# Kernel optimization log

Hardware: AMD Instinct MI355X
Metric: run time of the kernel (lower is better)

The kernel has to match this reference:

```python
import jax, jax.numpy as jnp
import numpy as np

NEG_INF = -1.0e9  # matches torch masked_fill value (unused: no mask)

def setup_inputs() -> dict:
    key = jax.random.key(0)
    kq, kk, kv = jax.random.split(key, 3)
    B, Sq, Sk, D = 8, 2048, 2048, 512
    return {
        "query": jax.random.normal(kq, (B, Sq, D), dtype=jnp.float32),
        "key": jax.random.normal(kk, (B, Sk, D), dtype=jnp.float32),
        "value": jax.random.normal(kv, (B, Sk, D), dtype=jnp.float32),
        "temperature": jnp.ones((), dtype=jnp.float32),
    }

def reference(query, key, value, temperature):
    # Squared Euclidean distance via GEMM identity: ||q||^2 + ||k||^2 - 2 q.k
    # (same math as the broadcast sum((q-k)^2, -1), but without [B,Sq,Sk,D] tensor)
    q_sq = jnp.sum(query * query, axis=-1, keepdims=True)          # [B,Sq,1]
    k_sq = jnp.sum(key * key, axis=-1)[:, None, :]                 # [B,1,Sk]
    qk = jnp.einsum("bqd,bkd->bqk", query, key)                    # [B,Sq,Sk]
    distance_squared = q_sq + k_sq - 2.0 * qk
    similarity = -distance_squared / temperature
    attention_weights = jax.nn.softmax(similarity, axis=-1)        # [B,Sq,Sk]
    attended_values = jnp.einsum("bqk,bkd->bqd", attention_weights, value)
    return attended_values, attention_weights
```

## Files before the change

kernel.cpp:

```cpp
#include <hip/hip_runtime.h>

typedef __bf16 bf16_t;
typedef __bf16 bf16x8 __attribute__((ext_vector_type(8)));
typedef __bf16 bf16x4 __attribute__((ext_vector_type(4)));
typedef __bf16 bf16x2 __attribute__((ext_vector_type(2)));
typedef float f32x4 __attribute__((ext_vector_type(4)));

#define NB 8
#define SQ 2048
#define SK 2048
#define DD 512

#define BM 128
#define BN 128
#define BK 32
#define LDK 40
#define NBLK (SK / BN)

__global__ __launch_bounds__(256, 2) void logits_kernel(
    const float* __restrict__ Q, const float* __restrict__ K,
    const float* __restrict__ tempP, float* __restrict__ logits,
    float* __restrict__ Mpart, float* __restrict__ Spart) {
  __shared__ bf16_t qh[BM][LDK], ql[BM][LDK], kh[BN][LDK], kl[BN][LDK];
  __shared__ float ksred[BN][8];
  __shared__ float mred[BM][2], sred[BM][2];
  const int b = blockIdx.z;
  const int m0 = blockIdx.y * BM;
  const int n0 = blockIdx.x * BN;
  const int tid = threadIdx.x;
  const int lane = tid & 63;
  const int wave = tid >> 6;
  const int wm = (wave >> 1) * 64;
  const int wn = (wave & 1) * 64;
  const int lrow = lane & 15;
  const int quad = lane >> 4;

  const float* Qb = Q + (size_t)b * SQ * DD;
  const float* Kb = K + (size_t)b * SK * DD;

  const int srow = tid >> 3;
  const int scol = (tid & 7) * 4;

  const float* qbase = Qb + (size_t)(m0 + srow) * DD + scol;
  const float* kbase = Kb + (size_t)(n0 + srow) * DD + scol;

  f32x4 acc[4][4];
#pragma unroll
  for (int i = 0; i < 4; i++)
#pragma unroll
    for (int j = 0; j < 4; j++) acc[i][j] = (f32x4){0.f, 0.f, 0.f, 0.f};

  float kss[4] = {0.f, 0.f, 0.f, 0.f};

  float4 pq[4], pk[4];
#pragma unroll
  for (int i = 0; i < 4; i++) {
    pq[i] = *(const float4*)(qbase + (size_t)i * 32 * DD);
    pk[i] = *(const float4*)(kbase + (size_t)i * 32 * DD);
  }

  for (int k0 = 0; k0 < DD; k0 += BK) {
    __syncthreads();
#pragma unroll
    for (int i = 0; i < 4; i++) {
      const int r = srow + i * 32;
      float4 qv = pq[i], kv = pk[i];
      bf16_t q0 = (bf16_t)qv.x, q1 = (bf16_t)qv.y, q2 = (bf16_t)qv.z, q3 = (bf16_t)qv.w;
      bf16x4 qhv = {q0, q1, q2, q3};
      bf16x4 qlv = {(bf16_t)(qv.x - (float)q0), (bf16_t)(qv.y - (float)q1),
                    (bf16_t)(qv.z - (float)q2), (bf16_t)(qv.w - (float)q3)};
      bf16_t c0 = (bf16_t)kv.x, c1 = (bf16_t)kv.y, c2 = (bf16_t)kv.z, c3 = (bf16_t)kv.w;
      bf16x4 khv = {c0, c1, c2, c3};
      bf16x4 klv = {(bf16_t)(kv.x - (float)c0), (bf16_t)(kv.y - (float)c1),
                    (bf16_t)(kv.z - (float)c2), (bf16_t)(kv.w - (float)c3)};
      *(bf16x4*)&qh[r][scol] = qhv;
      *(bf16x4*)&ql[r][scol] = qlv;
      *(bf16x4*)&kh[r][scol] = khv;
      *(bf16x4*)&kl[r][scol] = klv;
      kss[i] = fmaf(kv.x, kv.x, kss[i]);
      kss[i] = fmaf(kv.y, kv.y, kss[i]);
      kss[i] = fmaf(kv.z, kv.z, kss[i]);
      kss[i] = fmaf(kv.w, kv.w, kss[i]);
    }
    __syncthreads();

    if (k0 + BK < DD) {
#pragma unroll
      for (int i = 0; i < 4; i++) {
        pq[i] = *(const float4*)(qbase + (size_t)i * 32 * DD + (k0 + BK));
        pk[i] = *(const float4*)(kbase + (size_t)i * 32 * DD + (k0 + BK));
      }
    }

    bf16x8 bh[4], bl[4];
#pragma unroll
    for (int ni = 0; ni < 4; ni++) {
      bh[ni] = *(const bf16x8*)&kh[wn + ni * 16 + lrow][quad * 8];
      bl[ni] = *(const bf16x8*)&kl[wn + ni * 16 + lrow][quad * 8];
    }
#pragma unroll
    for (int mi = 0; mi < 4; mi++) {
      bf16x8 ah = *(const bf16x8*)&qh[wm + mi * 16 + lrow][quad * 8];
      bf16x8 al = *(const bf16x8*)&ql[wm + mi * 16 + lrow][quad * 8];
#pragma unroll
      for (int ni = 0; ni < 4; ni++) {
        acc[mi][ni] = __builtin_amdgcn_mfma_f32_16x16x32_bf16(ah, bh[ni], acc[mi][ni], 0, 0, 0);
        acc[mi][ni] = __builtin_amdgcn_mfma_f32_16x16x32_bf16(ah, bl[ni], acc[mi][ni], 0, 0, 0);
        acc[mi][ni] = __builtin_amdgcn_mfma_f32_16x16x32_bf16(al, bh[ni], acc[mi][ni], 0, 0, 0);
      }
    }
  }

#pragma unroll
  for (int i = 0; i < 4; i++) ksred[srow + i * 32][tid & 7] = kss[i];
  __syncthreads();

  const float invT = 1.4426950408889634f / tempP[0];
  float* Lb = logits + (size_t)b * SQ * SK;
  float ks4[4];
#pragma unroll
  for (int ni = 0; ni < 4; ni++) {
    const float* kr = ksred[wn + ni * 16 + lrow];
    ks4[ni] = ((kr[0] + kr[1]) + (kr[2] + kr[3])) +
              ((kr[4] + kr[5]) + (kr[6] + kr[7]));
  }

#pragma unroll
  for (int mi = 0; mi < 4; mi++) {
#pragma unroll
    for (int r = 0; r < 4; r++) {
      const int row = wm + mi * 16 + quad * 4 + r;
      float sv[4];
#pragma unroll
      for (int ni = 0; ni < 4; ni++) {
        sv[ni] = (2.0f * acc[mi][ni][r] - ks4[ni]) * invT;
        Lb[(size_t)(m0 + row) * SK + (n0 + wn + ni * 16 + lrow)] = sv[ni];
      }
      float rm = fmaxf(fmaxf(sv[0], sv[1]), fmaxf(sv[2], sv[3]));
      rm = fmaxf(rm, __shfl_xor(rm, 1));
      rm = fmaxf(rm, __shfl_xor(rm, 2));
      rm = fmaxf(rm, __shfl_xor(rm, 4));
      rm = fmaxf(rm, __shfl_xor(rm, 8));
      float rs = exp2f(sv[0] - rm) + exp2f(sv[1] - rm) +
                 exp2f(sv[2] - rm) + exp2f(sv[3] - rm);
      rs += __shfl_xor(rs, 1);
      rs += __shfl_xor(rs, 2);
      rs += __shfl_xor(rs, 4);
      rs += __shfl_xor(rs, 8);
      if (lrow == 0) {
        mred[row][wave & 1] = rm;
        sred[row][wave & 1] = rs;
      }
    }
  }
  __syncthreads();
  if (tid < BM) {
    const float ma = mred[tid][0], mb = mred[tid][1];
    const float M = fmaxf(ma, mb);
    const float S = sred[tid][0] * exp2f(ma - M) + sred[tid][1] * exp2f(mb - M);
    const size_t o = ((size_t)b * NBLK + blockIdx.x) * SQ + (m0 + tid);
    Mpart[o] = M;
    Spart[o] = S;
  }
}

__global__ __launch_bounds__(256) void vt_kernel(const float* __restrict__ V,
                                                 bf16_t* __restrict__ Vt) {
  const int b = blockIdx.y;
  const int k0 = blockIdx.x * 32;
  const int tid = threadIdx.x;
  const int p = tid & 15;
  const int c = tid >> 4;
  const float* Vb = V + (size_t)b * SK * DD;
  bf16_t* Vtb = Vt + (size_t)b * DD * SK;
  const int k = k0 + 2 * p;
#pragma unroll
  for (int j = 0; j < 8; j++) {
    const int d0 = 4 * c + 64 * j;
    float4 v0 = *(const float4*)(Vb + (size_t)k * DD + d0);
    float4 v1 = *(const float4*)(Vb + (size_t)(k + 1) * DD + d0);
    bf16x2 t0 = {(bf16_t)v0.x, (bf16_t)v1.x};
    bf16x2 t1 = {(bf16_t)v0.y, (bf16_t)v1.y};
    bf16x2 t2 = {(bf16_t)v0.z, (bf16_t)v1.z};
    bf16x2 t3 = {(bf16_t)v0.w, (bf16_t)v1.w};
    *(bf16x2*)(Vtb + (size_t)(d0 + 0) * SK + k) = t0;
    *(bf16x2*)(Vtb + (size_t)(d0 + 1) * SK + k) = t1;
    *(bf16x2*)(Vtb + (size_t)(d0 + 2) * SK + k) = t2;
    *(bf16x2*)(Vtb + (size_t)(d0 + 3) * SK + k) = t3;
  }
}

#define PM 32
#define CK 256
#define CKB 512
#define NCH (SK / CK)
#define NWIN (SK / BK)

__device__ __forceinline__ unsigned pv_lds(int row, unsigned kb) {
  return (unsigned)row * CKB + (kb ^ (unsigned)((row & 7) << 4));
}

__global__ __launch_bounds__(512, 4) void pv_kernel(
    float* __restrict__ L,
    const bf16_t* __restrict__ Vt,
    const float* __restrict__ Mpart, const float* __restrict__ Spart,
    float* __restrict__ O) {
  __shared__ __align__(16) unsigned char wlds[2][PM * CKB];
  __shared__ float Msh[PM], Ssh[PM];
  const int bid = blockIdx.x;
  const int b = bid & 7;
  const int m0 = (bid >> 3) * PM;
  const int tid = threadIdx.x;

  float* Lb = L + (size_t)b * SQ * SK;
  const bf16_t* Vtb = Vt + (size_t)b * DD * SK;

  {
    const int row = tid >> 4;
    const int j = tid & 15;
    const size_t o = ((size_t)b * NBLK + j) * SQ + (m0 + row);
    const float pm = Mpart[o];
    const float ps = Spart[o];
    float m = pm;
    m = fmaxf(m, __shfl_xor(m, 1));
    m = fmaxf(m, __shfl_xor(m, 2));
    m = fmaxf(m, __shfl_xor(m, 4));
    m = fmaxf(m, __shfl_xor(m, 8));
    float s = ps * exp2f(pm - m);
    s += __shfl_xor(s, 1);
    s += __shfl_xor(s, 2);
    s += __shfl_xor(s, 4);
    s += __shfl_xor(s, 8);
    if (j == 0) {
      Msh[row] = m;
      Ssh[row] = 1.0f / s;
    }
  }
  __syncthreads();

  const int prow = tid >> 4;
  const int g = tid & 15;
  float* lp = Lb + (size_t)(m0 + prow) * SK;
  const float Mrow = Msh[prow];
  const float invS = Ssh[prow];

  auto stage = [&](const float4 (&pv4)[4], int c1) {
    unsigned char* buf = wlds[c1 & 1];
    const int kbase = c1 * CK;
#pragma unroll
    for (int j = 0; j < 4; j++) {
      const int k = g * 4 + j * 64;
      float4 v = pv4[j];
      const float w0 = exp2f(v.x - Mrow) * invS;
      const float w1 = exp2f(v.y - Mrow) * invS;
      const float w2 = exp2f(v.z - Mrow) * invS;
      const float w3 = exp2f(v.w - Mrow) * invS;
      *(float4*)(lp + kbase + k) = make_float4(w0, w1, w2, w3);
      bf16x4 w4 = {(bf16_t)w0, (bf16_t)w1, (bf16_t)w2, (bf16_t)w3};
      *(bf16x4*)(buf + pv_lds(prow, (unsigned)(k * 2))) = w4;
    }
  };

  const int lane = tid & 63;
  const int wave = tid >> 6;
  const int wn = wave * 64;
  const int lrow = lane & 15;
  const int quad = lane >> 4;

  const bf16_t* Brow[4];
#pragma unroll
  for (int ni = 0; ni < 4; ni++)
    Brow[ni] = Vtb + (size_t)(wn + ni * 16 + lrow) * SK + quad * 8;

  f32x4 acc[2][4];
#pragma unroll
  for (int i = 0; i < 2; i++)
#pragma unroll
    for (int j = 0; j < 4; j++) acc[i][j] = (f32x4){0.f, 0.f, 0.f, 0.f};

  {
    float4 p0[4];
#pragma unroll
    for (int j = 0; j < 4; j++) p0[j] = *(const float4*)(lp + g * 4 + j * 64);
    stage(p0, 0);
  }
  bf16x8 bw[2][4];
#pragma unroll
  for (int ni = 0; ni < 4; ni++) bw[0][ni] = *(const bf16x8*)(Brow[ni]);
#pragma unroll
  for (int ni = 0; ni < 4; ni++) bw[1][ni] = *(const bf16x8*)(Brow[ni] + BK);
  __syncthreads();

  for (int c = 0; c < NCH; c++) {
    float4 pn[4];
    if (c + 1 < NCH) {
      const int kbase = (c + 1) * CK;
#pragma unroll
      for (int j = 0; j < 4; j++)
        pn[j] = *(const float4*)(lp + kbase + g * 4 + j * 64);
    }

    const unsigned char* buf = wlds[c & 1];
#pragma unroll
    for (int w = 0; w < CK / BK; w++) {
      const int gw = c * (CK / BK) + w;
      bf16x8 a0 = *(const bf16x8*)(buf + pv_lds(lrow, (unsigned)(w * 64 + quad * 16)));
      bf16x8 a1 = *(const bf16x8*)(buf + pv_lds(16 + lrow, (unsigned)(w * 64 + quad * 16)));
#pragma unroll
      for (int ni = 0; ni < 4; ni++)
        acc[0][ni] = __builtin_amdgcn_mfma_f32_16x16x32_bf16(a0, bw[gw & 1][ni],
                                                             acc[0][ni], 0, 0, 0);
#pragma unroll
      for (int ni = 0; ni < 4; ni++)
        acc[1][ni] = __builtin_amdgcn_mfma_f32_16x16x32_bf16(a1, bw[gw & 1][ni],
                                                             acc[1][ni], 0, 0, 0);
      if (gw + 2 < NWIN) {
#pragma unroll
        for (int ni = 0; ni < 4; ni++)
          bw[gw & 1][ni] = *(const bf16x8*)(Brow[ni] + (gw + 2) * BK);
      }
    }

    if (c + 1 < NCH) {
      stage(pn, c + 1);
      asm volatile("s_waitcnt lgkmcnt(0)\n\ts_barrier" ::: "memory");
    }
  }

  float* Ob = O + (size_t)b * SQ * DD;
#pragma unroll
  for (int ni = 0; ni < 4; ni++) {
    const int d = wn + ni * 16 + lrow;
#pragma unroll
    for (int mi = 0; mi < 2; mi++) {
      const int mbase = m0 + mi * 16 + quad * 4;
#pragma unroll
      for (int r = 0; r < 4; r++) {
        Ob[(size_t)(mbase + r) * DD + d] = acc[mi][ni][r];
      }
    }
  }
}

extern "C" void kernel_launch(void* const* d_in, const int* in_sizes, int n_in,
                              void* d_out, int out_size, void* d_ws, size_t ws_size,
                              hipStream_t stream) {
  const float* Q = (const float*)d_in[0];
  const float* K = (const float*)d_in[1];
  const float* V = (const float*)d_in[2];
  const float* T = (const float*)d_in[3];

  float* outv = (float*)d_out;
  float* logits = outv + (size_t)NB * SQ * DD;

  float* Mpart = (float*)d_ws;
  float* Spart = Mpart + (size_t)NB * NBLK * SQ;
  bf16_t* Vt = (bf16_t*)(Spart + (size_t)NB * NBLK * SQ);

  vt_kernel<<<dim3(SK / 32, NB), 256, 0, stream>>>(V, Vt);
  logits_kernel<<<dim3(SK / BN, SQ / BM, NB), 256, 0, stream>>>(Q, K, T, logits,
                                                                Mpart, Spart);
  pv_kernel<<<dim3(NB * (SQ / PM)), 512, 0, stream>>>(logits, Vt, Mpart, Spart, outv);
}
```

Before: 460.0 us.

## Pre-pack Q/K into bf16 hi/lo rows and deepen P·V logits prefetch

Adds a pack kernel that splits Q and K once into bf16 hi/lo halves in a workspace and precomputes the K row norms. The logits GEMM then streams the packed bf16 data as a single K-extended dimension of 1536 (hi·hi, hi·lo, lo·hi), instead of reloading fp32 and re-splitting it in every tile. This removes the conversion work repeated across the 16 tile columns and halves the bytes loaded per element, at the cost of an extra kernel and workspace traffic. The P·V kernel now prefetches logits two chunks ahead and unrolls the V window double-buffer into explicit registers.

```diff
diff --git a/kernel.cpp b/kernel.cpp
--- a/kernel.cpp
+++ b/kernel.cpp
@@ -10,6 +10,8 @@
 #define SQ 2048
 #define SK 2048
 #define DD 512
+#define KP2 1024
+#define KV 1536
 
 #define BM 128
 #define BN 128
@@ -17,12 +19,48 @@
 #define LDK 40
 #define NBLK (SK / BN)
 
+__global__ __launch_bounds__(256) void pack_kernel(
+    const float* __restrict__ Q, const float* __restrict__ K,
+    bf16_t* __restrict__ QP, bf16_t* __restrict__ KP, float* __restrict__ Ksq) {
+  const int row = blockIdx.x * 4 + (threadIdx.x >> 6);
+  const int lane = threadIdx.x & 63;
+  const float* q = Q + (size_t)row * DD;
+  const float* k = K + (size_t)row * DD;
+  bf16_t* qp = QP + (size_t)row * KP2;
+  bf16_t* kp = KP + (size_t)row * KP2;
+  float ks = 0.f;
+#pragma unroll
+  for (int j = 0; j < 2; j++) {
+    const int c = lane * 4 + j * 256;
+    float4 qv = *(const float4*)(q + c);
+    float4 kv = *(const float4*)(k + c);
+    bf16_t q0 = (bf16_t)qv.x, q1 = (bf16_t)qv.y, q2 = (bf16_t)qv.z, q3 = (bf16_t)qv.w;
+    bf16x4 qh = {q0, q1, q2, q3};
+    bf16x4 ql = {(bf16_t)(qv.x - (float)q0), (bf16_t)(qv.y - (float)q1),
+                 (bf16_t)(qv.z - (float)q2), (bf16_t)(qv.w - (float)q3)};
+    bf16_t c0 = (bf16_t)kv.x, c1 = (bf16_t)kv.y, c2 = (bf16_t)kv.z, c3 = (bf16_t)kv.w;
+    bf16x4 kh = {c0, c1, c2, c3};
+    bf16x4 kl = {(bf16_t)(kv.x - (float)c0), (bf16_t)(kv.y - (float)c1),
+                 (bf16_t)(kv.z - (float)c2), (bf16_t)(kv.w - (float)c3)};
+    *(bf16x4*)(qp + c) = qh;
+    *(bf16x4*)(qp + 512 + c) = ql;
+    *(bf16x4*)(kp + c) = kh;
+    *(bf16x4*)(kp + 512 + c) = kl;
+    ks = fmaf(kv.x, kv.x, ks);
+    ks = fmaf(kv.y, kv.y, ks);
+    ks = fmaf(kv.z, kv.z, ks);
+    ks = fmaf(kv.w, kv.w, ks);
+  }
+#pragma unroll
+  for (int off = 32; off; off >>= 1) ks += __shfl_xor(ks, off);
+  if (lane == 0) Ksq[row] = ks;
+}
+
 __global__ __launch_bounds__(256, 2) void logits_kernel(
-    const float* __restrict__ Q, const float* __restrict__ K,
-    const float* __restrict__ tempP, float* __restrict__ logits,
-    float* __restrict__ Mpart, float* __restrict__ Spart) {
-  __shared__ bf16_t qh[BM][LDK], ql[BM][LDK], kh[BN][LDK], kl[BN][LDK];
-  __shared__ float ksred[BN][8];
+    const bf16_t* __restrict__ QP, const bf16_t* __restrict__ KPp,
+    const float* __restrict__ Ksq, const float* __restrict__ tempP,
+    float* __restrict__ logits, float* __restrict__ Mpart, float* __restrict__ Spart) {
+  __shared__ bf16_t at[BM][LDK], bt[BN][LDK];
   __shared__ float mred[BM][2], sred[BM][2];
   const int b = blockIdx.z;
   const int m0 = blockIdx.y * BM;
@@ -35,14 +73,11 @@
   const int lrow = lane & 15;
   const int quad = lane >> 4;
 
-  const float* Qb = Q + (size_t)b * SQ * DD;
-  const float* Kb = K + (size_t)b * SK * DD;
-
-  const int srow = tid >> 3;
-  const int scol = (tid & 7) * 4;
-
-  const float* qbase = Qb + (size_t)(m0 + srow) * DD + scol;
-  const float* kbase = Kb + (size_t)(n0 + srow) * DD + scol;
+  const int srow = tid >> 1;
+  const int k8 = (tid & 1) * 8;
+
+  const bf16_t* qbase = QP + ((size_t)b * SQ + m0 + srow) * KP2 + k8;
+  const bf16_t* kbase = KPp + ((size_t)b * SK + n0 + srow) * KP2 + k8;
 
   f32x4 acc[4][4];
 #pragma unroll
@@ -50,80 +85,48 @@
 #pragma unroll
     for (int j = 0; j < 4; j++) acc[i][j] = (f32x4){0.f, 0.f, 0.f, 0.f};
 
-  float kss[4] = {0.f, 0.f, 0.f, 0.f};
-
-  float4 pq[4], pk[4];
-#pragma unroll
-  for (int i = 0; i < 4; i++) {
-    pq[i] = *(const float4*)(qbase + (size_t)i * 32 * DD);
-    pk[i] = *(const float4*)(kbase + (size_t)i * 32 * DD);
-  }
-
-  for (int k0 = 0; k0 < DD; k0 += BK) {
+  bf16x8 pa0 = *(const bf16x8*)(qbase);
+  bf16x8 pa1 = *(const bf16x8*)(qbase + 16);
+  bf16x8 pb0 = *(const bf16x8*)(kbase);
+  bf16x8 pb1 = *(const bf16x8*)(kbase + 16);
+
+  for (int kv = 0; kv < KV; kv += BK) {
     __syncthreads();
-#pragma unroll
-    for (int i = 0; i < 4; i++) {
-      const int r = srow + i * 32;
-      float4 qv = pq[i], kv = pk[i];
-      bf16_t q0 = (bf16_t)qv.x, q1 = (bf16_t)qv.y, q2 = (bf16_t)qv.z, q3 = (bf16_t)qv.w;
-      bf16x4 qhv = {q0, q1, q2, q3};
-      bf16x4 qlv = {(bf16_t)(qv.x - (float)q0), (bf16_t)(qv.y - (float)q1),
-                    (bf16_t)(qv.z - (float)q2), (bf16_t)(qv.w - (float)q3)};
-      bf16_t c0 = (bf16_t)kv.x, c1 = (bf16_t)kv.y, c2 = (bf16_t)kv.z, c3 = (bf16_t)kv.w;
-      bf16x4 khv = {c0, c1, c2, c3};
-      bf16x4 klv = {(bf16_t)(kv.x - (float)c0), (bf16_t)(kv.y - (float)c1),
-                    (bf16_t)(kv.z - (float)c2), (bf16_t)(kv.w - (float)c3)};
-      *(bf16x4*)&qh[r][scol] = qhv;
-      *(bf16x4*)&ql[r][scol] = qlv;
-      *(bf16x4*)&kh[r][scol] = khv;
-      *(bf16x4*)&kl[r][scol] = klv;
-      kss[i] = fmaf(kv.x, kv.x, kss[i]);
-      kss[i] = fmaf(kv.y, kv.y, kss[i]);
-      kss[i] = fmaf(kv.z, kv.z, kss[i]);
-      kss[i] = fmaf(kv.w, kv.w, kss[i]);
-    }
+    *(bf16x8*)&at[srow][k8] = pa0;
+    *(bf16x8*)&at[srow][k8 + 16] = pa1;
+    *(bf16x8*)&bt[srow][k8] = pb0;
+    *(bf16x8*)&bt[srow][k8 + 16] = pb1;
     __syncthreads();
 
-    if (k0 + BK < DD) {
-#pragma unroll
-      for (int i = 0; i < 4; i++) {
-        pq[i] = *(const float4*)(qbase + (size_t)i * 32 * DD + (k0 + BK));
-        pk[i] = *(const float4*)(kbase + (size_t)i * 32 * DD + (k0 + BK));
-      }
-    }
-
-    bf16x8 bh[4], bl[4];
-#pragma unroll
-    for (int ni = 0; ni < 4; ni++) {
-      bh[ni] = *(const bf16x8*)&kh[wn + ni * 16 + lrow][quad * 8];
-      bl[ni] = *(const bf16x8*)&kl[wn + ni * 16 + lrow][quad * 8];
-    }
+    if (kv + BK < KV) {
+      const int kn = kv + BK;
+      const int ao = (kn < 512) ? kn : kn - 512;
+      const int bo = (kn < 1024) ? kn : kn - 1024;
+      pa0 = *(const bf16x8*)(qbase + ao);
+      pa1 = *(const bf16x8*)(qbase + ao + 16);
+      pb0 = *(const bf16x8*)(kbase + bo);
+      pb1 = *(const bf16x8*)(kbase + bo + 16);
+    }
+
+    bf16x8 bfr[4];
+#pragma unroll
+    for (int ni = 0; ni < 4; ni++)
+      bfr[ni] = *(const bf16x8*)&bt[wn + ni * 16 + lrow][quad * 8];
 #pragma unroll
     for (int mi = 0; mi < 4; mi++) {
-      bf16x8 ah = *(const bf16x8*)&qh[wm + mi * 16 + lrow][quad * 8];
-      bf16x8 al = *(const bf16x8*)&ql[wm + mi * 16 + lrow][quad * 8];
-#pragma unroll
-      for (int ni = 0; ni < 4; ni++) {
-        acc[mi][ni] = __builtin_amdgcn_mfma_f32_16x16x32_bf16(ah, bh[ni], acc[mi][ni], 0, 0, 0);
-        acc[mi][ni] = __builtin_amdgcn_mfma_f32_16x16x32_bf16(ah, bl[ni], acc[mi][ni], 0, 0, 0);
-        acc[mi][ni] = __builtin_amdgcn_mfma_f32_16x16x32_bf16(al, bh[ni], acc[mi][ni], 0, 0, 0);
-      }
-    }
-  }
-
-#pragma unroll
-  for (int i = 0; i < 4; i++) ksred[srow + i * 32][tid & 7] = kss[i];
-  __syncthreads();
+      bf16x8 a = *(const bf16x8*)&at[wm + mi * 16 + lrow][quad * 8];
+#pragma unroll
+      for (int ni = 0; ni < 4; ni++)
+        acc[mi][ni] = __builtin_amdgcn_mfma_f32_16x16x32_bf16(a, bfr[ni], acc[mi][ni], 0, 0, 0);
+    }
+  }
 
   const float invT = 1.4426950408889634f / tempP[0];
   float* Lb = logits + (size_t)b * SQ * SK;
+  const float* ksb = Ksq + (size_t)b * SK + n0;
   float ks4[4];
 #pragma unroll
-  for (int ni = 0; ni < 4; ni++) {
-    const float* kr = ksred[wn + ni * 16 + lrow];
-    ks4[ni] = ((kr[0] + kr[1]) + (kr[2] + kr[3])) +
-              ((kr[4] + kr[5]) + (kr[6] + kr[7]));
-  }
+  for (int ni = 0; ni < 4; ni++) ks4[ni] = ksb[wn + ni * 16 + lrow];
 
 #pragma unroll
   for (int mi = 0; mi < 4; mi++) {
@@ -284,47 +287,68 @@
     for (int j = 0; j < 4; j++) p0[j] = *(const float4*)(lp + g * 4 + j * 64);
     stage(p0, 0);
   }
-  bf16x8 bw[2][4];
-#pragma unroll
-  for (int ni = 0; ni < 4; ni++) bw[0][ni] = *(const bf16x8*)(Brow[ni]);
-#pragma unroll
-  for (int ni = 0; ni < 4; ni++) bw[1][ni] = *(const bf16x8*)(Brow[ni] + BK);
+  float4 pA[4];
+#pragma unroll
+  for (int j = 0; j < 4; j++) pA[j] = *(const float4*)(lp + CK + g * 4 + j * 64);
+
+  bf16x8 bw0[4], bw1[4];
+#pragma unroll
+  for (int ni = 0; ni < 4; ni++) bw0[ni] = *(const bf16x8*)(Brow[ni]);
+#pragma unroll
+  for (int ni = 0; ni < 4; ni++) bw1[ni] = *(const bf16x8*)(Brow[ni] + BK);
   __syncthreads();
 
   for (int c = 0; c < NCH; c++) {
-    float4 pn[4];
+    float4 pB_[4] = {};
+    if (c + 2 < NCH) {
+      const int kbase = (c + 2) * CK;
+#pragma unroll
+      for (int j = 0; j < 4; j++)
+        pB_[j] = *(const float4*)(lp + kbase + g * 4 + j * 64);
+    }
+
+    const unsigned char* buf = wlds[c & 1];
+#pragma unroll
+    for (int w = 0; w < CK / BK; w += 2) {
+      const int gw = c * (CK / BK) + w;
+      {
+        bf16x8 a0 = *(const bf16x8*)(buf + pv_lds(lrow, (unsigned)(w * 64 + quad * 16)));
+        bf16x8 a1 = *(const bf16x8*)(buf + pv_lds(16 + lrow, (unsigned)(w * 64 + quad * 16)));
+#pragma unroll
+        for (int ni = 0; ni < 4; ni++)
+          acc[0][ni] = __builtin_amdgcn_mfma_f32_16x16x32_bf16(a0, bw0[ni], acc[0][ni], 0, 0, 0);
+#pragma unroll
+        for (int ni = 0; ni < 4; ni++)
+          acc[1][ni] = __builtin_amdgcn_mfma_f32_16x16x32_bf16(a1, bw0[ni], acc[1][ni], 0, 0, 0);
+        if (gw + 2 < NWIN) {
+#pragma unroll
+          for (int ni = 0; ni < 4; ni++)
+            bw0[ni] = *(const bf16x8*)(Brow[ni] + (gw + 2) * BK);
+        }
+      }
+      {
+        bf16x8 a0 = *(const bf16x8*)(buf + pv_lds(lrow, (unsigned)((w + 1) * 64 + quad * 16)));
+        bf16x8 a1 = *(const bf16x8*)(buf + pv_lds(16 + lrow, (unsigned)((w + 1) * 64 + quad * 16)));
+#pragma unroll
+        for (int ni = 0; ni < 4; ni++)
+          acc[0][ni] = __builtin_amdgcn_mfma_f32_16x16x32_bf16(a0, bw1[ni], acc[0][ni], 0, 0, 0);
+#pragma unroll
+        for (int ni = 0; ni < 4; ni++)
+          acc[1][ni] = __builtin_amdgcn_mfma_f32_16x16x32_bf16(a1, bw1[ni], acc[1][ni], 0, 0, 0);
+        if (gw + 3 < NWIN) {
+#pragma unroll
+          for (int ni = 0; ni < 4; ni++)
+            bw1[ni] = *(const bf16x8*)(Brow[ni] + (gw + 3) * BK);
+        }
+      }
+    }
+
     if (c + 1 < NCH) {
-      const int kbase = (c + 1) * CK;
-#pragma unroll
-      for (int j = 0; j < 4; j++)
-        pn[j] = *(const float4*)(lp + kbase + g * 4 + j * 64);
-    }
-
-    const unsigned char* buf = wlds[c & 1];
-#pragma unroll
-    for (int w = 0; w < CK / BK; w++) {
-      const int gw = c * (CK / BK) + w;
-      bf16x8 a0 = *(const bf16x8*)(buf + pv_lds(lrow, (unsigned)(w * 64 + quad * 16)));
-      bf16x8 a1 = *(const bf16x8*)(buf + pv_lds(16 + lrow, (unsigned)(w * 64 + quad * 16)));
-#pragma unroll
-      for (int ni = 0; ni < 4; ni++)
-        acc[0][ni] = __builtin_amdgcn_mfma_f32_16x16x32_bf16(a0, bw[gw & 1][ni],
-                                                             acc[0][ni], 0, 0, 0);
-#pragma unroll
-      for (int ni = 0; ni < 4; ni++)
-        acc[1][ni] = __builtin_amdgcn_mfma_f32_16x16x32_bf16(a1, bw[gw & 1][ni],
-                                                             acc[1][ni], 0, 0, 0);
-      if (gw + 2 < NWIN) {
-#pragma unroll
-        for (int ni = 0; ni < 4; ni++)
-          bw[gw & 1][ni] = *(const bf16x8*)(Brow[ni] + (gw + 2) * BK);
-      }
-    }
-
-    if (c + 1 < NCH) {
-      stage(pn, c + 1);
+      stage(pA, c + 1);
       asm volatile("s_waitcnt lgkmcnt(0)\n\ts_barrier" ::: "memory");
     }
+#pragma unroll
+    for (int j = 0; j < 4; j++) pA[j] = pB_[j];
   }
 
   float* Ob = O + (size_t)b * SQ * DD;
@@ -356,9 +380,13 @@
   float* Mpart = (float*)d_ws;
   float* Spart = Mpart + (size_t)NB * NBLK * SQ;
   bf16_t* Vt = (bf16_t*)(Spart + (size_t)NB * NBLK * SQ);
-
+  bf16_t* QP = Vt + (size_t)NB * DD * SK;
+  bf16_t* KPp = QP + (size_t)NB * SQ * KP2;
+  float* Ksq = (float*)(KPp + (size_t)NB * SK * KP2);
+
+  pack_kernel<<<NB * SQ / 4, 256, 0, stream>>>(Q, K, QP, KPp, Ksq);
   vt_kernel<<<dim3(SK / 32, NB), 256, 0, stream>>>(V, Vt);
-  logits_kernel<<<dim3(SK / BN, SQ / BM, NB), 256, 0, stream>>>(Q, K, T, logits,
-                                                                Mpart, Spart);
+  logits_kernel<<<dim3(SK / BN, SQ / BM, NB), 256, 0, stream>>>(QP, KPp, Ksq, T,
+                                                                logits, Mpart, Spart);
   pv_kernel<<<dim3(NB * (SQ / PM)), 512, 0, stream>>>(logits, Vt, Mpart, Spart, outv);
 }
```

New measurement: 510.0 us. 10.9% more time.

## Drop V transpose kernel and partial softmax stats; convert V in-kernel and recompute stats

Applied to the files above, without the earlier changes.

Removes the separate V transpose/bf16 conversion kernel and the per-block max/sum partials from the logits kernel. The PV kernel now first re-reads each logits row to compute the online softmax max and sum itself. It then loads fp32 V tiles per 32-key window, converts and transposes them into a padded LDS buffer, and feeds them to MFMA. This saves a launch, the Vt workspace round trip and the epilogue reductions. In exchange it adds an extra full read of the logits, with each block re-reading and converting all of V. It also adds two barriers per 32-key window.

```diff
diff --git a/kernel.cpp b/kernel.cpp
--- a/kernel.cpp
+++ b/kernel.cpp
@@ -15,15 +15,12 @@
 #define BN 128
 #define BK 32
 #define LDK 40
-#define NBLK (SK / BN)
 
 __global__ __launch_bounds__(256, 2) void logits_kernel(
     const float* __restrict__ Q, const float* __restrict__ K,
-    const float* __restrict__ tempP, float* __restrict__ logits,
-    float* __restrict__ Mpart, float* __restrict__ Spart) {
+    const float* __restrict__ tempP, float* __restrict__ logits) {
   __shared__ bf16_t qh[BM][LDK], ql[BM][LDK], kh[BN][LDK], kl[BN][LDK];
   __shared__ float ksred[BN][8];
-  __shared__ float mred[BM][2], sred[BM][2];
   const int b = blockIdx.z;
   const int m0 = blockIdx.y * BM;
   const int n0 = blockIdx.x * BN;
@@ -130,63 +127,12 @@
 #pragma unroll
     for (int r = 0; r < 4; r++) {
       const int row = wm + mi * 16 + quad * 4 + r;
-      float sv[4];
 #pragma unroll
       for (int ni = 0; ni < 4; ni++) {
-        sv[ni] = (2.0f * acc[mi][ni][r] - ks4[ni]) * invT;
-        Lb[(size_t)(m0 + row) * SK + (n0 + wn + ni * 16 + lrow)] = sv[ni];
-      }
-      float rm = fmaxf(fmaxf(sv[0], sv[1]), fmaxf(sv[2], sv[3]));
-      rm = fmaxf(rm, __shfl_xor(rm, 1));
-      rm = fmaxf(rm, __shfl_xor(rm, 2));
-      rm = fmaxf(rm, __shfl_xor(rm, 4));
-      rm = fmaxf(rm, __shfl_xor(rm, 8));
-      float rs = exp2f(sv[0] - rm) + exp2f(sv[1] - rm) +
-                 exp2f(sv[2] - rm) + exp2f(sv[3] - rm);
-      rs += __shfl_xor(rs, 1);
-      rs += __shfl_xor(rs, 2);
-      rs += __shfl_xor(rs, 4);
-      rs += __shfl_xor(rs, 8);
-      if (lrow == 0) {
-        mred[row][wave & 1] = rm;
-        sred[row][wave & 1] = rs;
-      }
-    }
-  }
-  __syncthreads();
-  if (tid < BM) {
-    const float ma = mred[tid][0], mb = mred[tid][1];
-    const float M = fmaxf(ma, mb);
-    const float S = sred[tid][0] * exp2f(ma - M) + sred[tid][1] * exp2f(mb - M);
-    const size_t o = ((size_t)b * NBLK + blockIdx.x) * SQ + (m0 + tid);
-    Mpart[o] = M;
-    Spart[o] = S;
-  }
-}
-
-__global__ __launch_bounds__(256) void vt_kernel(const float* __restrict__ V,
-                                                 bf16_t* __restrict__ Vt) {
-  const int b = blockIdx.y;
-  const int k0 = blockIdx.x * 32;
-  const int tid = threadIdx.x;
-  const int p = tid & 15;
-  const int c = tid >> 4;
-  const float* Vb = V + (size_t)b * SK * DD;
-  bf16_t* Vtb = Vt + (size_t)b * DD * SK;
-  const int k = k0 + 2 * p;
-#pragma unroll
-  for (int j = 0; j < 8; j++) {
-    const int d0 = 4 * c + 64 * j;
-    float4 v0 = *(const float4*)(Vb + (size_t)k * DD + d0);
-    float4 v1 = *(const float4*)(Vb + (size_t)(k + 1) * DD + d0);
-    bf16x2 t0 = {(bf16_t)v0.x, (bf16_t)v1.x};
-    bf16x2 t1 = {(bf16_t)v0.y, (bf16_t)v1.y};
-    bf16x2 t2 = {(bf16_t)v0.z, (bf16_t)v1.z};
-    bf16x2 t3 = {(bf16_t)v0.w, (bf16_t)v1.w};
-    *(bf16x2*)(Vtb + (size_t)(d0 + 0) * SK + k) = t0;
-    *(bf16x2*)(Vtb + (size_t)(d0 + 1) * SK + k) = t1;
-    *(bf16x2*)(Vtb + (size_t)(d0 + 2) * SK + k) = t2;
-    *(bf16x2*)(Vtb + (size_t)(d0 + 3) * SK + k) = t3;
+        float sv = (2.0f * acc[mi][ni][r] - ks4[ni]) * invT;
+        Lb[(size_t)(m0 + row) * SK + (n0 + wn + ni * 16 + lrow)] = sv;
+      }
+    }
   }
 }
 
@@ -194,7 +140,7 @@
 #define CK 256
 #define CKB 512
 #define NCH (SK / CK)
-#define NWIN (SK / BK)
+#define LDV 40
 
 __device__ __forceinline__ unsigned pv_lds(int row, unsigned kb) {
   return (unsigned)row * CKB + (kb ^ (unsigned)((row & 7) << 4));
@@ -202,10 +148,10 @@
 
 __global__ __launch_bounds__(512, 4) void pv_kernel(
     float* __restrict__ L,
-    const bf16_t* __restrict__ Vt,
-    const float* __restrict__ Mpart, const float* __restrict__ Spart,
+    const float* __restrict__ V,
     float* __restrict__ O) {
   __shared__ __align__(16) unsigned char wlds[2][PM * CKB];
+  __shared__ __align__(16) bf16_t vwin[DD][LDV];
   __shared__ float Msh[PM], Ssh[PM];
   const int bid = blockIdx.x;
   const int b = bid & 7;
@@ -213,44 +159,55 @@
   const int tid = threadIdx.x;
 
   float* Lb = L + (size_t)b * SQ * SK;
-  const bf16_t* Vtb = Vt + (size_t)b * DD * SK;
-
-  {
-    const int row = tid >> 4;
-    const int j = tid & 15;
-    const size_t o = ((size_t)b * NBLK + j) * SQ + (m0 + row);
-    const float pm = Mpart[o];
-    const float ps = Spart[o];
-    float m = pm;
-    m = fmaxf(m, __shfl_xor(m, 1));
-    m = fmaxf(m, __shfl_xor(m, 2));
-    m = fmaxf(m, __shfl_xor(m, 4));
-    m = fmaxf(m, __shfl_xor(m, 8));
-    float s = ps * exp2f(pm - m);
-    s += __shfl_xor(s, 1);
-    s += __shfl_xor(s, 2);
-    s += __shfl_xor(s, 4);
-    s += __shfl_xor(s, 8);
-    if (j == 0) {
-      Msh[row] = m;
-      Ssh[row] = 1.0f / s;
-    }
-  }
-  __syncthreads();
+  const float* Vb = V + (size_t)b * SK * DD;
 
   const int prow = tid >> 4;
   const int g = tid & 15;
   float* lp = Lb + (size_t)(m0 + prow) * SK;
+
+  {
+    float ma = -3.0e38f, sa = 0.f, mb2 = -3.0e38f, sb = 0.f;
+#pragma unroll 4
+    for (int j = 0; j < 32; j += 2) {
+      float4 v = *(const float4*)(lp + g * 4 + j * 64);
+      float4 u = *(const float4*)(lp + g * 4 + (j + 1) * 64);
+      float mv = fmaxf(fmaxf(v.x, v.y), fmaxf(v.z, v.w));
+      float mn = fmaxf(ma, mv);
+      sa = sa * exp2f(ma - mn) + (exp2f(v.x - mn) + exp2f(v.y - mn)) +
+           (exp2f(v.z - mn) + exp2f(v.w - mn));
+      ma = mn;
+      float mu = fmaxf(fmaxf(u.x, u.y), fmaxf(u.z, u.w));
+      float mo = fmaxf(mb2, mu);
+      sb = sb * exp2f(mb2 - mo) + (exp2f(u.x - mo) + exp2f(u.y - mo)) +
+           (exp2f(u.z - mo) + exp2f(u.w - mo));
+      mb2 = mo;
+    }
+    float m = fmaxf(ma, mb2);
+    float s = sa * exp2f(ma - m) + sb * exp2f(mb2 - m);
+#pragma unroll
+    for (int off = 1; off <= 8; off <<= 1) {
+      float mo = __shfl_xor(m, off);
+      float so = __shfl_xor(s, off);
+      float mm = fmaxf(m, mo);
+      s = s * exp2f(m - mm) + so * exp2f(mo - mm);
+      m = mm;
+    }
+    if (g == 0) {
+      Msh[prow] = m;
+      Ssh[prow] = 1.0f / s;
+    }
+  }
+  __syncthreads();
   const float Mrow = Msh[prow];
   const float invS = Ssh[prow];
 
-  auto stage = [&](const float4 (&pv4)[4], int c1) {
+  auto stageW = [&](const float4 (&pw)[4], int c1) {
     unsigned char* buf = wlds[c1 & 1];
     const int kbase = c1 * CK;
 #pragma unroll
     for (int j = 0; j < 4; j++) {
       const int k = g * 4 + j * 64;
-      float4 v = pv4[j];
+      float4 v = pw[j];
       const float w0 = exp2f(v.x - Mrow) * invS;
       const float w1 = exp2f(v.y - Mrow) * invS;
       const float w2 = exp2f(v.z - Mrow) * invS;
@@ -261,17 +218,16 @@
     }
   };
 
+  const int p = tid & 15;
+  const int c2 = tid >> 4;
+  const float* vk = Vb + (size_t)(2 * p) * DD + 4 * c2;
+
   const int lane = tid & 63;
   const int wave = tid >> 6;
   const int wn = wave * 64;
   const int lrow = lane & 15;
   const int quad = lane >> 4;
 
-  const bf16_t* Brow[4];
-#pragma unroll
-  for (int ni = 0; ni < 4; ni++)
-    Brow[ni] = Vtb + (size_t)(wn + ni * 16 + lrow) * SK + quad * 8;
-
   f32x4 acc[2][4];
 #pragma unroll
   for (int i = 0; i < 2; i++)
@@ -282,48 +238,68 @@
     float4 p0[4];
 #pragma unroll
     for (int j = 0; j < 4; j++) p0[j] = *(const float4*)(lp + g * 4 + j * 64);
-    stage(p0, 0);
-  }
-  bf16x8 bw[2][4];
-#pragma unroll
-  for (int ni = 0; ni < 4; ni++) bw[0][ni] = *(const bf16x8*)(Brow[ni]);
-#pragma unroll
-  for (int ni = 0; ni < 4; ni++) bw[1][ni] = *(const bf16x8*)(Brow[ni] + BK);
-  __syncthreads();
+    stageW(p0, 0);
+  }
+  float4 pw[4];
+#pragma unroll
+  for (int j = 0; j < 4; j++) pw[j] = *(const float4*)(lp + CK + g * 4 + j * 64);
+
+  float4 va[4], vb2[4];
+#pragma unroll
+  for (int j = 0; j < 4; j++) {
+    va[j] = *(const float4*)(vk + 128 * j);
+    vb2[j] = *(const float4*)(vk + DD + 128 * j);
+  }
 
   for (int c = 0; c < NCH; c++) {
-    float4 pn[4];
+    const unsigned char* buf = wlds[c & 1];
+#pragma unroll
+    for (int wloc = 0; wloc < CK / BK; wloc++) {
+      const int gw = c * (CK / BK) + wloc;
+      __builtin_amdgcn_s_barrier();
+#pragma unroll
+      for (int j = 0; j < 4; j++) {
+        const int d0 = 4 * c2 + 128 * j;
+        float4 a0 = va[j], a1 = vb2[j];
+        bf16x2 t0 = {(bf16_t)a0.x, (bf16_t)a1.x};
+        bf16x2 t1 = {(bf16_t)a0.y, (bf16_t)a1.y};
+        bf16x2 t2 = {(bf16_t)a0.z, (bf16_t)a1.z};
+        bf16x2 t3 = {(bf16_t)a0.w, (bf16_t)a1.w};
+        *(bf16x2*)&vwin[d0 + 0][2 * p] = t0;
+        *(bf16x2*)&vwin[d0 + 1][2 * p] = t1;
+        *(bf16x2*)&vwin[d0 + 2][2 * p] = t2;
+        *(bf16x2*)&vwin[d0 + 3][2 * p] = t3;
+      }
+      asm volatile("s_waitcnt lgkmcnt(0)\n\ts_barrier" ::: "memory");
+      if (gw + 1 < SK / BK) {
+        const float* vn = vk + (size_t)(gw + 1) * BK * DD;
+#pragma unroll
+        for (int j = 0; j < 4; j++) {
+          va[j] = *(const float4*)(vn + 128 * j);
+          vb2[j] = *(const float4*)(vn + DD + 128 * j);
+        }
+      }
+      bf16x8 bb[4];
+#pragma unroll
+      for (int ni = 0; ni < 4; ni++)
+        bb[ni] = *(const bf16x8*)&vwin[wn + ni * 16 + lrow][quad * 8];
+      bf16x8 a0 = *(const bf16x8*)(buf + pv_lds(lrow, (unsigned)(wloc * 64 + quad * 16)));
+      bf16x8 a1 = *(const bf16x8*)(buf + pv_lds(16 + lrow, (unsigned)(wloc * 64 + quad * 16)));
+#pragma unroll
+      for (int ni = 0; ni < 4; ni++)
+        acc[0][ni] = __builtin_amdgcn_mfma_f32_16x16x32_bf16(a0, bb[ni], acc[0][ni], 0, 0, 0);
+#pragma unroll
+      for (int ni = 0; ni < 4; ni++)
+        acc[1][ni] = __builtin_amdgcn_mfma_f32_16x16x32_bf16(a1, bb[ni], acc[1][ni], 0, 0, 0);
+    }
     if (c + 1 < NCH) {
-      const int kbase = (c + 1) * CK;
-#pragma unroll
-      for (int j = 0; j < 4; j++)
-        pn[j] = *(const float4*)(lp + kbase + g * 4 + j * 64);
-    }
-
-    const unsigned char* buf = wlds[c & 1];
-#pragma unroll
-    for (int w = 0; w < CK / BK; w++) {
-      const int gw = c * (CK / BK) + w;
-      bf16x8 a0 = *(const bf16x8*)(buf + pv_lds(lrow, (unsigned)(w * 64 + quad * 16)));
-      bf16x8 a1 = *(const bf16x8*)(buf + pv_lds(16 + lrow, (unsigned)(w * 64 + quad * 16)));
-#pragma unroll
-      for (int ni = 0; ni < 4; ni++)
-        acc[0][ni] = __builtin_amdgcn_mfma_f32_16x16x32_bf16(a0, bw[gw & 1][ni],
-                                                             acc[0][ni], 0, 0, 0);
-#pragma unroll
-      for (int ni = 0; ni < 4; ni++)
-        acc[1][ni] = __builtin_amdgcn_mfma_f32_16x16x32_bf16(a1, bw[gw & 1][ni],
-                                                             acc[1][ni], 0, 0, 0);
-      if (gw + 2 < NWIN) {
-#pragma unroll
-        for (int ni = 0; ni < 4; ni++)
-          bw[gw & 1][ni] = *(const bf16x8*)(Brow[ni] + (gw + 2) * BK);
-      }
-    }
-
-    if (c + 1 < NCH) {
-      stage(pn, c + 1);
-      asm volatile("s_waitcnt lgkmcnt(0)\n\ts_barrier" ::: "memory");
+      stageW(pw, c + 1);
+      if (c + 2 < NCH) {
+        const int kbase = (c + 2) * CK;
+#pragma unroll
+        for (int j = 0; j < 4; j++)
+          pw[j] = *(const float4*)(lp + kbase + g * 4 + j * 64);
+      }
     }
   }
 
@@ -353,12 +329,6 @@
   float* outv = (float*)d_out;
   float* logits = outv + (size_t)NB * SQ * DD;
 
-  float* Mpart = (float*)d_ws;
-  float* Spart = Mpart + (size_t)NB * NBLK * SQ;
-  bf16_t* Vt = (bf16_t*)(Spart + (size_t)NB * NBLK * SQ);
-
-  vt_kernel<<<dim3(SK / 32, NB), 256, 0, stream>>>(V, Vt);
-  logits_kernel<<<dim3(SK / BN, SQ / BM, NB), 256, 0, stream>>>(Q, K, T, logits,
-                                                                Mpart, Spart);
-  pv_kernel<<<dim3(NB * (SQ / PM)), 512, 0, stream>>>(logits, Vt, Mpart, Spart, outv);
+  logits_kernel<<<dim3(SK / BN, SQ / BM, NB), 256, 0, stream>>>(Q, K, T, logits);
+  pv_kernel<<<dim3(NB * (SQ / PM)), 512, 0, stream>>>(logits, V, outv);
 }
```

Measured after the change: 595.2 us. 29.4% more time.

## Store local exponentials in logits pass and rescale per group in PV pass

Applied to the files above, without the earlier changes.

The logits kernel now writes exp2(s - local_max) per 64-column wave group instead of raw logits, and emits per-wave partial max/sum directly, dropping the block-level LDS reduction and barrier. The PV kernel merges 32 partials with an online-softmax shuffle reduction, precomputes a per-row, per-group scale factor in shared memory, and turns the exp2 on every weight into a single multiply. It also deepens the logits prefetch to two chunks ahead and splits the V register double-buffer into two named arrays. This moves transcendental work out of the memory-bound PV pass, at the cost of extra exp work in the logits epilogue, twice as many partials, and more registers.

```diff
diff --git a/kernel.cpp b/kernel.cpp
--- a/kernel.cpp
+++ b/kernel.cpp
@@ -15,7 +15,7 @@
 #define BN 128
 #define BK 32
 #define LDK 40
-#define NBLK (SK / BN)
+#define NG 32
 
 __global__ __launch_bounds__(256, 2) void logits_kernel(
     const float* __restrict__ Q, const float* __restrict__ K,
@@ -23,7 +23,6 @@
     float* __restrict__ Mpart, float* __restrict__ Spart) {
   __shared__ bf16_t qh[BM][LDK], ql[BM][LDK], kh[BN][LDK], kl[BN][LDK];
   __shared__ float ksred[BN][8];
-  __shared__ float mred[BM][2], sred[BM][2];
   const int b = blockIdx.z;
   const int m0 = blockIdx.y * BM;
   const int n0 = blockIdx.x * BN;
@@ -125,6 +124,8 @@
               ((kr[4] + kr[5]) + (kr[6] + kr[7]));
   }
 
+  const size_t gbase = ((size_t)b * NG + blockIdx.x * 2 + (wave & 1)) * SQ + m0;
+
 #pragma unroll
   for (int mi = 0; mi < 4; mi++) {
 #pragma unroll
@@ -132,35 +133,30 @@
       const int row = wm + mi * 16 + quad * 4 + r;
       float sv[4];
 #pragma unroll
-      for (int ni = 0; ni < 4; ni++) {
+      for (int ni = 0; ni < 4; ni++)
         sv[ni] = (2.0f * acc[mi][ni][r] - ks4[ni]) * invT;
-        Lb[(size_t)(m0 + row) * SK + (n0 + wn + ni * 16 + lrow)] = sv[ni];
-      }
       float rm = fmaxf(fmaxf(sv[0], sv[1]), fmaxf(sv[2], sv[3]));
       rm = fmaxf(rm, __shfl_xor(rm, 1));
       rm = fmaxf(rm, __shfl_xor(rm, 2));
       rm = fmaxf(rm, __shfl_xor(rm, 4));
       rm = fmaxf(rm, __shfl_xor(rm, 8));
-      float rs = exp2f(sv[0] - rm) + exp2f(sv[1] - rm) +
-                 exp2f(sv[2] - rm) + exp2f(sv[3] - rm);
+      float e[4];
+      float rs = 0.f;
+#pragma unroll
+      for (int ni = 0; ni < 4; ni++) {
+        e[ni] = exp2f(sv[ni] - rm);
+        rs += e[ni];
+        Lb[(size_t)(m0 + row) * SK + (n0 + wn + ni * 16 + lrow)] = e[ni];
+      }
       rs += __shfl_xor(rs, 1);
       rs += __shfl_xor(rs, 2);
       rs += __shfl_xor(rs, 4);
       rs += __shfl_xor(rs, 8);
       if (lrow == 0) {
-        mred[row][wave & 1] = rm;
-        sred[row][wave & 1] = rs;
-      }
-    }
-  }
-  __syncthreads();
-  if (tid < BM) {
-    const float ma = mred[tid][0], mb = mred[tid][1];
-    const float M = fmaxf(ma, mb);
-    const float S = sred[tid][0] * exp2f(ma - M) + sred[tid][1] * exp2f(mb - M);
-    const size_t o = ((size_t)b * NBLK + blockIdx.x) * SQ + (m0 + tid);
-    Mpart[o] = M;
-    Spart[o] = S;
+        Mpart[gbase + row] = rm;
+        Spart[gbase + row] = rs;
+      }
+    }
   }
 }
 
@@ -206,6 +202,7 @@
     const float* __restrict__ Mpart, const float* __restrict__ Spart,
     float* __restrict__ O) {
   __shared__ __align__(16) unsigned char wlds[2][PM * CKB];
+  __shared__ float ash[PM][NG];
   __shared__ float Msh[PM], Ssh[PM];
   const int bid = blockIdx.x;
   const int b = bid & 7;
@@ -215,46 +212,52 @@
   float* Lb = L + (size_t)b * SQ * SK;
   const bf16_t* Vtb = Vt + (size_t)b * DD * SK;
 
-  {
-    const int row = tid >> 4;
-    const int j = tid & 15;
-    const size_t o = ((size_t)b * NBLK + j) * SQ + (m0 + row);
-    const float pm = Mpart[o];
-    const float ps = Spart[o];
-    float m = pm;
-    m = fmaxf(m, __shfl_xor(m, 1));
-    m = fmaxf(m, __shfl_xor(m, 2));
-    m = fmaxf(m, __shfl_xor(m, 4));
-    m = fmaxf(m, __shfl_xor(m, 8));
-    float s = ps * exp2f(pm - m);
-    s += __shfl_xor(s, 1);
-    s += __shfl_xor(s, 2);
-    s += __shfl_xor(s, 4);
-    s += __shfl_xor(s, 8);
-    if (j == 0) {
-      Msh[row] = m;
-      Ssh[row] = 1.0f / s;
-    }
-  }
-  __syncthreads();
-
   const int prow = tid >> 4;
   const int g = tid & 15;
+  {
+    const size_t o = ((size_t)b * NG + g) * SQ + (m0 + prow);
+    const float pm0 = Mpart[o], ps0 = Spart[o];
+    const float pm1 = Mpart[o + (size_t)16 * SQ], ps1 = Spart[o + (size_t)16 * SQ];
+    float m = fmaxf(pm0, pm1);
+    float s = ps0 * exp2f(pm0 - m) + ps1 * exp2f(pm1 - m);
+#pragma unroll
+    for (int off = 1; off <= 8; off <<= 1) {
+      float mo = __shfl_xor(m, off);
+      float so = __shfl_xor(s, off);
+      float mm = fmaxf(m, mo);
+      s = s * exp2f(m - mm) + so * exp2f(mo - mm);
+      m = mm;
+    }
+    if (g == 0) {
+      Msh[prow] = m;
+      Ssh[prow] = 1.0f / s;
+    }
+    __syncthreads();
+    const float M = Msh[prow];
+    const float invS = Ssh[prow];
+    ash[prow][g] = exp2f(pm0 - M) * invS;
+    ash[prow][g + 16] = exp2f(pm1 - M) * invS;
+  }
+  __syncthreads();
+
   float* lp = Lb + (size_t)(m0 + prow) * SK;
-  const float Mrow = Msh[prow];
-  const float invS = Ssh[prow];
-
-  auto stage = [&](const float4 (&pv4)[4], int c1) {
+
+  auto stageW = [&](const float4 (&pw)[4], int c1) {
     unsigned char* buf = wlds[c1 & 1];
     const int kbase = c1 * CK;
+    float a0 = ash[prow][c1 * 4 + 0];
+    float a1 = ash[prow][c1 * 4 + 1];
+    float a2 = ash[prow][c1 * 4 + 2];
+    float a3 = ash[prow][c1 * 4 + 3];
+    const float aj[4] = {a0, a1, a2, a3};
 #pragma unroll
     for (int j = 0; j < 4; j++) {
       const int k = g * 4 + j * 64;
-      float4 v = pv4[j];
-      const float w0 = exp2f(v.x - Mrow) * invS;
-      const float w1 = exp2f(v.y - Mrow) * invS;
-      const float w2 = exp2f(v.z - Mrow) * invS;
-      const float w3 = exp2f(v.w - Mrow) * invS;
+      float4 v = pw[j];
+      const float w0 = v.x * aj[j];
+      const float w1 = v.y * aj[j];
+      const float w2 = v.z * aj[j];
+      const float w3 = v.w * aj[j];
       *(float4*)(lp + kbase + k) = make_float4(w0, w1, w2, w3);
       bf16x4 w4 = {(bf16_t)w0, (bf16_t)w1, (bf16_t)w2, (bf16_t)w3};
       *(bf16x4*)(buf + pv_lds(prow, (unsigned)(k * 2))) = w4;
@@ -282,49 +285,70 @@
     float4 p0[4];
 #pragma unroll
     for (int j = 0; j < 4; j++) p0[j] = *(const float4*)(lp + g * 4 + j * 64);
-    stage(p0, 0);
-  }
-  bf16x8 bw[2][4];
-#pragma unroll
-  for (int ni = 0; ni < 4; ni++) bw[0][ni] = *(const bf16x8*)(Brow[ni]);
-#pragma unroll
-  for (int ni = 0; ni < 4; ni++) bw[1][ni] = *(const bf16x8*)(Brow[ni] + BK);
+    stageW(p0, 0);
+  }
+  float4 pA[4];
+#pragma unroll
+  for (int j = 0; j < 4; j++) pA[j] = *(const float4*)(lp + CK + g * 4 + j * 64);
+
+  bf16x8 bw0[4], bw1[4];
+#pragma unroll
+  for (int ni = 0; ni < 4; ni++) bw0[ni] = *(const bf16x8*)(Brow[ni]);
+#pragma unroll
+  for (int ni = 0; ni < 4; ni++) bw1[ni] = *(const bf16x8*)(Brow[ni] + BK);
   __syncthreads();
 
   for (int c = 0; c < NCH; c++) {
-    float4 pn[4];
+    float4 pB_[4] = {};
+    if (c + 2 < NCH) {
+      const int kbase = (c + 2) * CK;
+#pragma unroll
+      for (int j = 0; j < 4; j++)
+        pB_[j] = *(const float4*)(lp + kbase + g * 4 + j * 64);
+    }
+
+    const unsigned char* buf = wlds[c & 1];
+#pragma unroll
+    for (int w = 0; w < CK / BK; w += 2) {
+      const int gw = c * (CK / BK) + w;
+      {
+        bf16x8 a0 = *(const bf16x8*)(buf + pv_lds(lrow, (unsigned)(w * 64 + quad * 16)));
+        bf16x8 a1 = *(const bf16x8*)(buf + pv_lds(16 + lrow, (unsigned)(w * 64 + quad * 16)));
+#pragma unroll
+        for (int ni = 0; ni < 4; ni++)
+          acc[0][ni] = __builtin_amdgcn_mfma_f32_16x16x32_bf16(a0, bw0[ni], acc[0][ni], 0, 0, 0);
+#pragma unroll
+        for (int ni = 0; ni < 4; ni++)
+          acc[1][ni] = __builtin_amdgcn_mfma_f32_16x16x32_bf16(a1, bw0[ni], acc[1][ni], 0, 0, 0);
+        if (gw + 2 < NWIN) {
+#pragma unroll
+          for (int ni = 0; ni < 4; ni++)
+            bw0[ni] = *(const bf16x8*)(Brow[ni] + (gw + 2) * BK);
+        }
+      }
+      {
+        bf16x8 a0 = *(const bf16x8*)(buf + pv_lds(lrow, (unsigned)((w + 1) * 64 + quad * 16)));
+        bf16x8 a1 = *(const bf16x8*)(buf + pv_lds(16 + lrow, (unsigned)((w + 1) * 64 + quad * 16)));
+#pragma unroll
+        for (int ni = 0; ni < 4; ni++)
+          acc[0][ni] = __builtin_amdgcn_mfma_f32_16x16x32_bf16(a0, bw1[ni], acc[0][ni], 0, 0, 0);
+#pragma unroll
+        for (int ni = 0; ni < 4; ni++)
+          acc[1][ni] = __builtin_amdgcn_mfma_f32_16x16x32_bf16(a1, bw1[ni], acc[1][ni], 0, 0, 0);
+        if (gw + 3 < NWIN) {
+#pragma unroll
+          for (int ni = 0; ni < 4; ni++)
+            bw1[ni] = *(const bf16x8*)(Brow[ni] + (gw + 3) * BK);
+        }
+      }
+    }
+
     if (c + 1 < NCH) {
-      const int kbase = (c + 1) * CK;
-#pragma unroll
-      for (int j = 0; j < 4; j++)
-        pn[j] = *(const float4*)(lp + kbase + g * 4 + j * 64);
-    }
-
-    const unsigned char* buf = wlds[c & 1];
-#pragma unroll
-    for (int w = 0; w < CK / BK; w++) {
-      const int gw = c * (CK / BK) + w;
-      bf16x8 a0 = *(const bf16x8*)(buf + pv_lds(lrow, (unsigned)(w * 64 + quad * 16)));
-      bf16x8 a1 = *(const bf16x8*)(buf + pv_lds(16 + lrow, (unsigned)(w * 64 + quad * 16)));
-#pragma unroll
-      for (int ni = 0; ni < 4; ni++)
-        acc[0][ni] = __builtin_amdgcn_mfma_f32_16x16x32_bf16(a0, bw[gw & 1][ni],
-                                                             acc[0][ni], 0, 0, 0);
-#pragma unroll
-      for (int ni = 0; ni < 4; ni++)
-        acc[1][ni] = __builtin_amdgcn_mfma_f32_16x16x32_bf16(a1, bw[gw & 1][ni],
-                                                             acc[1][ni], 0, 0, 0);
-      if (gw + 2 < NWIN) {
-#pragma unroll
-        for (int ni = 0; ni < 4; ni++)
-          bw[gw & 1][ni] = *(const bf16x8*)(Brow[ni] + (gw + 2) * BK);
-      }
-    }
-
-    if (c + 1 < NCH) {
-      stage(pn, c + 1);
+      stageW(pA, c + 1);
       asm volatile("s_waitcnt lgkmcnt(0)\n\ts_barrier" ::: "memory");
     }
+#pragma unroll
+    for (int j = 0; j < 4; j++) pA[j] = pB_[j];
   }
 
   float* Ob = O + (size_t)b * SQ * DD;
@@ -354,8 +378,8 @@
   float* logits = outv + (size_t)NB * SQ * DD;
 
   float* Mpart = (float*)d_ws;
-  float* Spart = Mpart + (size_t)NB * NBLK * SQ;
-  bf16_t* Vt = (bf16_t*)(Spart + (size_t)NB * NBLK * SQ);
+  float* Spart = Mpart + (size_t)NB * NG * SQ;
+  bf16_t* Vt = (bf16_t*)(Spart + (size_t)NB * NG * SQ);
 
   vt_kernel<<<dim3(SK / 32, NB), 256, 0, stream>>>(V, Vt);
   logits_kernel<<<dim3(SK / BN, SQ / BM, NB), 256, 0, stream>>>(Q, K, T, logits,
```

New measurement: 489.6 us. +6.4%, slower.
